# Optimization experiments

Measured on AMD Instinct MI355X. Metric: run time of the kernel, lower is better.

## Reference

```python
import jax, jax.numpy as jnp
import numpy as np

NUM_HEADS = 16
HEAD_DIM = 64
SCALE = HEAD_DIM ** -0.5


def setup_inputs() -> dict:
    key = jax.random.key(0)
    ks = jax.random.split(key, 5)
    B, N, C = 2, 2048, 1024
    x = jax.random.normal(ks[0], (B, N, C), dtype=jnp.float32)
    rel_pos_bias = jax.random.normal(ks[1], (NUM_HEADS, N, N), dtype=jnp.float32) * 0.02
    qkv_w = jax.random.normal(ks[2], (3 * C, C), dtype=jnp.float32) * (C ** -0.5)
    q_bias = jnp.zeros((C,), dtype=jnp.float32)
    v_bias = jnp.zeros((C,), dtype=jnp.float32)
    proj_w = jax.random.normal(ks[3], (C, C), dtype=jnp.float32) * (C ** -0.5)
    proj_b = jnp.zeros((C,), dtype=jnp.float32)
    return {"x": x, "rel_pos_bias": rel_pos_bias, "qkv_w": qkv_w,
            "q_bias": q_bias, "v_bias": v_bias, "proj_w": proj_w, "proj_b": proj_b}


def reference(x, rel_pos_bias, qkv_w, q_bias, v_bias, proj_w, proj_b):
    B, N, C = x.shape
    H, D = NUM_HEADS, HEAD_DIM
    # qkv bias = concat(q_bias, zeros, v_bias)
    qkv_b = jnp.concatenate([q_bias, jnp.zeros_like(v_bias), v_bias])
    qkv = x @ qkv_w.T + qkv_b                       # [B, N, 3C]
    qkv = qkv.reshape(B, N, 3, H, D).transpose(2, 0, 3, 1, 4)  # [3, B, H, N, D]
    q, k, v = qkv[0], qkv[1], qkv[2]
    q = q * SCALE
    attn = jnp.einsum('bhnd,bhmd->bhnm', q, k)      # [B, H, N, N]
    attn = attn + rel_pos_bias[None]                # bias broadcast over batch
    attn = jax.nn.softmax(attn, axis=-1)
    out = jnp.einsum('bhnm,bhmd->bhnd', attn, v)    # [B, H, N, D]
    out = out.transpose(0, 2, 1, 3).reshape(B, N, H * D)
    out = out @ proj_w.T + proj_b
    return out
```

## Files before the change

### kernel.cpp

```cpp
#include <hip/hip_runtime.h>

typedef unsigned short u16;
typedef short bfrag __attribute__((ext_vector_type(8)));
typedef float facc  __attribute__((ext_vector_type(4)));

#define LOG2E 1.44269504088896340736f

static __device__ __forceinline__ float bf2f(u16 b) {
  union { unsigned u; float f; } v; v.u = ((unsigned)b) << 16; return v.f;
}
static __device__ __forceinline__ u16 f2bf(float x) {
  union { float f; unsigned u; } v; v.f = x;
  return (u16)((v.u + 0x7FFFu + ((v.u >> 16) & 1u)) >> 16);
}
static __device__ __forceinline__ void gload_lds16(const u16* g, u16* l) {
  __builtin_amdgcn_global_load_lds((const __attribute__((address_space(1))) void*)g,
                                   (__attribute__((address_space(3))) void*)l,
                                   16, 0, 0);
}

__global__ __launch_bounds__(256) void convert_kernel(
    const float* __restrict__ x, const float* __restrict__ qw, const float* __restrict__ pw,
    u16* __restrict__ xb, u16* __restrict__ qwb, u16* __restrict__ pwb)
{
  const int NX = 4 * 1024 * 1024, NQ = 3 * 1024 * 1024, NP = 1024 * 1024;
  const int total4 = (NX + NQ + NP) >> 2;
  for (int i = blockIdx.x * blockDim.x + threadIdx.x; i < total4;
       i += gridDim.x * blockDim.x) {
    const int e = i << 2;
    const float* s; u16* d; int off;
    if (e < NX)            { s = x;  d = xb;  off = e; }
    else if (e < NX + NQ)  { s = qw; d = qwb; off = e - NX; }
    else                   { s = pw; d = pwb; off = e - NX - NQ; }
    float4 v = *(const float4*)(s + off);
    ushort4 o;
    o.x = f2bf(v.x); o.y = f2bf(v.y); o.z = f2bf(v.z); o.w = f2bf(v.w);
    *(ushort4*)(d + off) = o;
  }
}

static __device__ __forceinline__ void gemm128_bt(
    const u16* __restrict__ A, const u16* __restrict__ B, int K,
    int m0, int n0, u16* As, u16* Bs, facc acc[4][4])
{
  const int lane = threadIdx.x & 63;
  const int wv   = threadIdx.x >> 6;
  const int quad = lane >> 4;
  const int l15  = lane & 15;
  const int wm = wv >> 1, wn = wv & 1;
  const int srow = lane >> 2;
  const int skb  = (lane & 3) * 8;

  facc zero = {0.f, 0.f, 0.f, 0.f};
#pragma unroll
  for (int i = 0; i < 4; ++i)
#pragma unroll
    for (int j = 0; j < 4; ++j) acc[i][j] = zero;

  const int nIter = K >> 5;
  for (int kk = 0; kk < nIter; ++kk) {
    const int k0 = kk << 5;
    __syncthreads();
#pragma unroll
    for (int c = 0; c < 2; ++c) {
      const int seg = wv * 2 + c;
      gload_lds16(A + (long)(m0 + seg * 16 + srow) * K + k0 + skb, As + seg * 512);
      gload_lds16(B + (long)(n0 + seg * 16 + srow) * K + k0 + skb, Bs + seg * 512);
    }
    __syncthreads();
    bfrag af[4], bf[4];
#pragma unroll
    for (int i = 0; i < 4; ++i)
      af[i] = *(const bfrag*)(As + (wm * 64 + i * 16 + l15) * 32 + quad * 8);
#pragma unroll
    for (int j = 0; j < 4; ++j)
      bf[j] = *(const bfrag*)(Bs + (wn * 64 + j * 16 + l15) * 32 + quad * 8);
#pragma unroll
    for (int i = 0; i < 4; ++i)
#pragma unroll
      for (int j = 0; j < 4; ++j)
        acc[i][j] = __builtin_amdgcn_mfma_f32_16x16x32_bf16(af[i], bf[j], acc[i][j], 0, 0, 0);
  }
}

__global__ __launch_bounds__(256) void qkv_gemm_kernel(
    const u16* __restrict__ x, const u16* __restrict__ w,
    const float* __restrict__ qb, const float* __restrict__ vb,
    u16* __restrict__ Q, u16* __restrict__ Kd, u16* __restrict__ Vt)
{
  __shared__ u16 As[128 * 32];
  __shared__ u16 Bs[128 * 32];
  facc acc[4][4];
  const int m0 = blockIdx.y * 128;
  const int n0 = blockIdx.x * 128;
  gemm128_bt(x, w, 1024, m0, n0, As, Bs, acc);

  const int lane = threadIdx.x & 63;
  const int wv = threadIdx.x >> 6;
  const int quad = lane >> 4, l15 = lane & 15;
  const int wm = wv >> 1, wn = wv & 1;
  const int ncb = n0 + wn * 64;
  const int which = ncb >> 10;
  const int h = (ncb >> 6) & 15;

#pragma unroll
  for (int j = 0; j < 4; ++j) {
    const int d = j * 16 + l15;
    const int n_g = ncb + d;
#pragma unroll
    for (int i = 0; i < 4; ++i) {
      const int mg0 = m0 + wm * 64 + i * 16 + quad * 4;
      const int b  = mg0 >> 11;
      const int ns = mg0 & 2047;
      if (which == 0) {
        const float qbv = qb[n_g];
#pragma unroll
        for (int r = 0; r < 4; ++r)
          Q[(((long)(b * 16 + h) * 2048 + ns + r) << 6) + d] =
              f2bf((acc[i][j][r] + qbv) * 0.125f);
      } else if (which == 1) {
#pragma unroll
        for (int r = 0; r < 4; ++r)
          Kd[(((long)(b * 16 + h) * 2048 + ns + r) << 6) + d] = f2bf(acc[i][j][r]);
      } else {
        const float vbv = vb[n_g - 2048];
        ushort4 pk;
        pk.x = f2bf(acc[i][j][0] + vbv);
        pk.y = f2bf(acc[i][j][1] + vbv);
        pk.z = f2bf(acc[i][j][2] + vbv);
        pk.w = f2bf(acc[i][j][3] + vbv);
        *(ushort4*)(Vt + (((long)((b * 16 + h) * 64 + d)) << 11) + ns) = pk;
      }
    }
  }
}

__global__ __launch_bounds__(256) void attn_kernel(
    const u16* __restrict__ Q, const u16* __restrict__ Kd, const u16* __restrict__ Vt,
    const float* __restrict__ bias, u16* __restrict__ AO)
{
  __shared__ u16 P[4][16 * 32];
  const int lane = threadIdx.x & 63;
  const int wv = threadIdx.x >> 6;
  const int quad = lane >> 4, l15 = lane & 15;
  const int bh = blockIdx.x >> 5;
  const int qt = blockIdx.x & 31;
  const int h = bh & 15;
  const int b = bh >> 4;
  const int q0 = qt * 64 + wv * 16;
  const long baseN = (long)bh << 17;

  bfrag qf0 = *(const bfrag*)(Q + baseN + (long)(q0 + l15) * 64 + quad * 8);
  bfrag qf1 = *(const bfrag*)(Q + baseN + (long)(q0 + l15) * 64 + 32 + quad * 8);

  facc o[4];
  float m_i[4], l_i[4];
  facc zero = {0.f, 0.f, 0.f, 0.f};
#pragma unroll
  for (int t = 0; t < 4; ++t) o[t] = zero;
#pragma unroll
  for (int r = 0; r < 4; ++r) { m_i[r] = -1e30f; l_i[r] = 0.f; }

  const float* brow = bias + ((long)h << 22) + ((long)q0 << 11);
  u16* Pw = &P[wv][0];

  for (int k0 = 0; k0 < 2048; k0 += 32) {
    facc s[2];
#pragma unroll
    for (int kt = 0; kt < 2; ++kt) {
      bfrag kf0 = *(const bfrag*)(Kd + baseN + (long)(k0 + kt * 16 + l15) * 64 + quad * 8);
      bfrag kf1 = *(const bfrag*)(Kd + baseN + (long)(k0 + kt * 16 + l15) * 64 + 32 + quad * 8);
      facc z = zero;
      z = __builtin_amdgcn_mfma_f32_16x16x32_bf16(qf0, kf0, z, 0, 0, 0);
      z = __builtin_amdgcn_mfma_f32_16x16x32_bf16(qf1, kf1, z, 0, 0, 0);
      s[kt] = z;
    }
#pragma unroll
    for (int kt = 0; kt < 2; ++kt)
#pragma unroll
      for (int r = 0; r < 4; ++r)
        s[kt][r] += brow[(long)(quad * 4 + r) * 2048 + k0 + kt * 16 + l15];

    float alpha[4];
#pragma unroll
    for (int r = 0; r < 4; ++r) {
      float v = fmaxf(s[0][r], s[1][r]);
      v = fmaxf(v, __shfl_xor(v, 1, 16));
      v = fmaxf(v, __shfl_xor(v, 2, 16));
      v = fmaxf(v, __shfl_xor(v, 4, 16));
      v = fmaxf(v, __shfl_xor(v, 8, 16));
      const float mn = fmaxf(m_i[r], v);
      alpha[r] = exp2f((m_i[r] - mn) * LOG2E);
      m_i[r] = mn;
    }
#pragma unroll
    for (int r = 0; r < 4; ++r) {
      const float p0 = exp2f((s[0][r] - m_i[r]) * LOG2E);
      const float p1 = exp2f((s[1][r] - m_i[r]) * LOG2E);
      s[0][r] = p0; s[1][r] = p1;
      float v = p0 + p1;
      v += __shfl_xor(v, 1, 16);
      v += __shfl_xor(v, 2, 16);
      v += __shfl_xor(v, 4, 16);
      v += __shfl_xor(v, 8, 16);
      l_i[r] = l_i[r] * alpha[r] + v;
    }
#pragma unroll
    for (int t = 0; t < 4; ++t)
#pragma unroll
      for (int r = 0; r < 4; ++r) o[t][r] *= alpha[r];

#pragma unroll
    for (int kt = 0; kt < 2; ++kt)
#pragma unroll
      for (int r = 0; r < 4; ++r)
        Pw[(quad * 4 + r) * 32 + kt * 16 + l15] = f2bf(s[kt][r]);
    __syncthreads();

    bfrag pf = *(const bfrag*)(Pw + l15 * 32 + quad * 8);
#pragma unroll
    for (int t = 0; t < 4; ++t) {
      bfrag vf = *(const bfrag*)(Vt + baseN + (((long)(t * 16 + l15)) << 11) + k0 + quad * 8);
      o[t] = __builtin_amdgcn_mfma_f32_16x16x32_bf16(pf, vf, o[t], 0, 0, 0);
    }
    __syncthreads();
  }

#pragma unroll
  for (int r = 0; r < 4; ++r) l_i[r] = 1.0f / l_i[r];
#pragma unroll
  for (int t = 0; t < 4; ++t)
#pragma unroll
    for (int r = 0; r < 4; ++r) {
      const int row = q0 + quad * 4 + r;
      AO[(((long)(b * 2048 + row)) << 10) + h * 64 + t * 16 + l15] = f2bf(o[t][r] * l_i[r]);
    }
}

__global__ __launch_bounds__(256) void proj_kernel(
    const u16* __restrict__ Ain, const u16* __restrict__ w,
    const float* __restrict__ pb, float* __restrict__ out)
{
  __shared__ u16 As[128 * 32];
  __shared__ u16 Bs[128 * 32];
  facc acc[4][4];
  const int m0 = blockIdx.y * 128;
  const int n0 = blockIdx.x * 128;
  gemm128_bt(Ain, w, 1024, m0, n0, As, Bs, acc);

  const int lane = threadIdx.x & 63;
  const int wv = threadIdx.x >> 6;
  const int quad = lane >> 4, l15 = lane & 15;
  const int wm = wv >> 1, wn = wv & 1;
#pragma unroll
  for (int j = 0; j < 4; ++j) {
    const int n_g = n0 + wn * 64 + j * 16 + l15;
    const float pbv = pb[n_g];
#pragma unroll
    for (int i = 0; i < 4; ++i) {
      const int mg0 = m0 + wm * 64 + i * 16 + quad * 4;
#pragma unroll
      for (int r = 0; r < 4; ++r)
        out[(((long)(mg0 + r)) << 10) + n_g] = acc[i][j][r] + pbv;
    }
  }
}

extern "C" void kernel_launch(void* const* d_in, const int* in_sizes, int n_in,
                              void* d_out, int out_size, void* d_ws, size_t ws_size,
                              hipStream_t stream)
{
  const float* x    = (const float*)d_in[0];
  const float* bias = (const float*)d_in[1];
  const float* qkvw = (const float*)d_in[2];
  const float* qb   = (const float*)d_in[3];
  const float* vb   = (const float*)d_in[4];
  const float* pw   = (const float*)d_in[5];
  const float* pb   = (const float*)d_in[6];
  float* out = (float*)d_out;

  char* ws = (char*)d_ws;
  u16* Q    = (u16*)(ws);
  u16* Kd   = (u16*)(ws + (size_t)8  * 1024 * 1024);
  u16* Vt   = (u16*)(ws + (size_t)16 * 1024 * 1024);
  u16* AO   = (u16*)(ws + (size_t)24 * 1024 * 1024);
  u16* xb   = (u16*)(ws + (size_t)32 * 1024 * 1024);
  u16* qwb  = (u16*)(ws + (size_t)40 * 1024 * 1024);
  u16* pwb  = (u16*)(ws + (size_t)46 * 1024 * 1024);

  hipLaunchKernelGGL(convert_kernel, dim3(1024), dim3(256), 0, stream,
                     x, qkvw, pw, xb, qwb, pwb);
  hipLaunchKernelGGL(qkv_gemm_kernel, dim3(24, 32), dim3(256), 0, stream,
                     xb, qwb, qb, vb, Q, Kd, Vt);
  hipLaunchKernelGGL(attn_kernel, dim3(1024), dim3(256), 0, stream,
                     Q, Kd, Vt, bias, AO);
  hipLaunchKernelGGL(proj_kernel, dim3(8, 32), dim3(256), 0, stream,
                     AO, pwb, pb, out);
}
```

Baseline: 642.1 us.

## Widen attention key tile to 64 and replace block barriers with wave barriers

Result: no change. 645.2 us (+0.5%).

```diff
diff --git a/kernel.cpp b/kernel.cpp
--- a/kernel.cpp
+++ b/kernel.cpp
@@ -1,4 +1,5 @@
 #include <hip/hip_runtime.h>
+#include <hip/hip_bf16.h>
 
 typedef unsigned short u16;
 typedef short bfrag __attribute__((ext_vector_type(8)));
@@ -6,9 +7,6 @@
 
 #define LOG2E 1.44269504088896340736f
 
-static __device__ __forceinline__ float bf2f(u16 b) {
-  union { unsigned u; float f; } v; v.u = ((unsigned)b) << 16; return v.f;
-}
 static __device__ __forceinline__ u16 f2bf(float x) {
   union { float f; unsigned u; } v; v.f = x;
   return (u16)((v.u + 0x7FFFu + ((v.u >> 16) & 1u)) >> 16);
@@ -139,7 +137,7 @@
     const u16* __restrict__ Q, const u16* __restrict__ Kd, const u16* __restrict__ Vt,
     const float* __restrict__ bias, u16* __restrict__ AO)
 {
-  __shared__ u16 P[4][16 * 32];
+  __shared__ u16 P[4][16 * 64];
   const int lane = threadIdx.x & 63;
   const int wv = threadIdx.x >> 6;
   const int quad = lane >> 4, l15 = lane & 15;
@@ -161,30 +159,46 @@
 #pragma unroll
   for (int r = 0; r < 4; ++r) { m_i[r] = -1e30f; l_i[r] = 0.f; }
 
-  const float* brow = bias + ((long)h << 22) + ((long)q0 << 11);
+  const u16*  kp   = Kd + baseN + (long)l15 * 64 + quad * 8;
+  const u16*  vp   = Vt + baseN + (long)l15 * 2048 + quad * 8;
+  const float* brow = bias + ((long)h << 22) + (long)(q0 + quad * 4) * 2048 + l15;
+
   u16* Pw = &P[wv][0];
-
-  for (int k0 = 0; k0 < 2048; k0 += 32) {
-    facc s[2];
-#pragma unroll
-    for (int kt = 0; kt < 2; ++kt) {
-      bfrag kf0 = *(const bfrag*)(Kd + baseN + (long)(k0 + kt * 16 + l15) * 64 + quad * 8);
-      bfrag kf1 = *(const bfrag*)(Kd + baseN + (long)(k0 + kt * 16 + l15) * 64 + 32 + quad * 8);
+  u16* pwr = Pw + (quad * 4) * 64 + l15;
+  const u16* pr0 = Pw + l15 * 64 + quad * 8;
+
+  for (int it = 0; it < 32; ++it) {
+    bfrag kf0[4], kf1[4];
+#pragma unroll
+    for (int kt = 0; kt < 4; ++kt) {
+      kf0[kt] = *(const bfrag*)(kp + kt * 1024);
+      kf1[kt] = *(const bfrag*)(kp + kt * 1024 + 32);
+    }
+    float bv[4][4];
+#pragma unroll
+    for (int kt = 0; kt < 4; ++kt)
+#pragma unroll
+      for (int r = 0; r < 4; ++r)
+        bv[kt][r] = brow[r * 2048 + kt * 16];
+
+    facc s[4];
+#pragma unroll
+    for (int kt = 0; kt < 4; ++kt) {
       facc z = zero;
-      z = __builtin_amdgcn_mfma_f32_16x16x32_bf16(qf0, kf0, z, 0, 0, 0);
-      z = __builtin_amdgcn_mfma_f32_16x16x32_bf16(qf1, kf1, z, 0, 0, 0);
+      z = __builtin_amdgcn_mfma_f32_16x16x32_bf16(qf0, kf0[kt], z, 0, 0, 0);
+      z = __builtin_amdgcn_mfma_f32_16x16x32_bf16(qf1, kf1[kt], z, 0, 0, 0);
       s[kt] = z;
     }
 #pragma unroll
-    for (int kt = 0; kt < 2; ++kt)
+    for (int kt = 0; kt < 4; ++kt)
 #pragma unroll
       for (int r = 0; r < 4; ++r)
-        s[kt][r] += brow[(long)(quad * 4 + r) * 2048 + k0 + kt * 16 + l15];
+        s[kt][r] += bv[kt][r];
 
     float alpha[4];
 #pragma unroll
     for (int r = 0; r < 4; ++r) {
-      float v = fmaxf(s[0][r], s[1][r]);
+      float v = fmaxf(fmaxf(s[0][r], s[1][r]), fmaxf(s[2][r], s[3][r]));
       v = fmaxf(v, __shfl_xor(v, 1, 16));
       v = fmaxf(v, __shfl_xor(v, 2, 16));
       v = fmaxf(v, __shfl_xor(v, 4, 16));
@@ -195,10 +209,11 @@
     }
 #pragma unroll
     for (int r = 0; r < 4; ++r) {
-      const float p0 = exp2f((s[0][r] - m_i[r]) * LOG2E);
-      const float p1 = exp2f((s[1][r] - m_i[r]) * LOG2E);
-      s[0][r] = p0; s[1][r] = p1;
-      float v = p0 + p1;
+      const float mr = m_i[r];
+#pragma unroll
+      for (int kt = 0; kt < 4; ++kt)
+        s[kt][r] = exp2f((s[kt][r] - mr) * LOG2E);
+      float v = (s[0][r] + s[1][r]) + (s[2][r] + s[3][r]);
       v += __shfl_xor(v, 1, 16);
       v += __shfl_xor(v, 2, 16);
       v += __shfl_xor(v, 4, 16);
@@ -211,19 +226,30 @@
       for (int r = 0; r < 4; ++r) o[t][r] *= alpha[r];
 
 #pragma unroll
-    for (int kt = 0; kt < 2; ++kt)
-#pragma unroll
-      for (int r = 0; r < 4; ++r)
-        Pw[(quad * 4 + r) * 32 + kt * 16 + l15] = f2bf(s[kt][r]);
-    __syncthreads();
-
-    bfrag pf = *(const bfrag*)(Pw + l15 * 32 + quad * 8);
+    for (int r = 0; r < 4; ++r) {
+      union { __hip_bfloat162 h; u16 u[2]; } c01, c23;
+      c01.h = __float22bfloat162_rn(make_float2(s[0][r], s[1][r]));
+      c23.h = __float22bfloat162_rn(make_float2(s[2][r], s[3][r]));
+      u16* pw = pwr + r * 64;
+      pw[0]  = c01.u[0]; pw[16] = c01.u[1];
+      pw[32] = c23.u[0]; pw[48] = c23.u[1];
+    }
+    __builtin_amdgcn_wave_barrier();
+
+    bfrag pf0 = *(const bfrag*)(pr0);
+    bfrag pf1 = *(const bfrag*)(pr0 + 32);
 #pragma unroll
     for (int t = 0; t < 4; ++t) {
-      bfrag vf = *(const bfrag*)(Vt + baseN + (((long)(t * 16 + l15)) << 11) + k0 + quad * 8);
-      o[t] = __builtin_amdgcn_mfma_f32_16x16x32_bf16(pf, vf, o[t], 0, 0, 0);
-    }
-    __syncthreads();
+      bfrag vf0 = *(const bfrag*)(vp + t * 32768);
+      bfrag vf1 = *(const bfrag*)(vp + t * 32768 + 32);
+      o[t] = __builtin_amdgcn_mfma_f32_16x16x32_bf16(pf0, vf0, o[t], 0, 0, 0);
+      o[t] = __builtin_amdgcn_mfma_f32_16x16x32_bf16(pf1, vf1, o[t], 0, 0, 0);
+    }
+    __builtin_amdgcn_wave_barrier();
+
+    kp += 64 * 64;
+    vp += 64;
+    brow += 64;
   }
 
 #pragma unroll
```
